# Kernel tuning notes

Measured on AMD Instinct MI355X. Metric: run time of the kernel, lower is better.

The kernel has to match this reference:

```python
import jax, jax.numpy as jnp
import numpy as np

NUM_EXPERTS = 64
TOP_K = 2
NOISE_EPS = 0.01


def setup_inputs() -> dict:
    key = jax.random.key(0)
    k1, k2, k3, k4 = jax.random.split(key, 4)
    B, D, E = 32768, 2048, NUM_EXPERTS
    x = jax.random.normal(k1, (B, D), dtype=jnp.float32)
    # original inits these to zero; use small random weights for a non-degenerate top-k
    w_gate = jax.random.normal(k2, (D, E), dtype=jnp.float32) * 0.02
    w_noise = jax.random.normal(k3, (D, E), dtype=jnp.float32) * 0.02
    noise = jax.random.normal(k4, (B, E), dtype=jnp.float32)  # tf.random.normal draw, fixed
    return {"x": x, "w_gate": w_gate, "w_noise": w_noise, "noise": noise}


def reference(x, w_gate, w_noise, noise):
    # routing_pooling='flatten' on a 2D input is identity
    pooled = x  # [B, D]
    routing = pooled @ w_gate  # [B, E]
    # noisy routing (training=True path)
    noise_stddev = jax.nn.softplus(pooled @ w_noise) + NOISE_EPS
    routing = routing + noise * noise_stddev
    # softmax_top_k: take top k+1, keep top k, softmax, scatter back to E experts
    kk = min(TOP_K + 1, NUM_EXPERTS)
    top_vals, top_idx = jax.lax.top_k(routing, kk)
    top_k_vals = top_vals[:, :TOP_K]            # [B, k]
    top_k_idx = top_idx[:, :TOP_K]              # [B, k]
    top_k_gates = jax.nn.softmax(top_k_vals, axis=-1)
    B = routing.shape[0]
    rows = jnp.arange(B)[:, None]
    # rowwise_unsorted_segment_sum -> scatter gates into expert slots
    out = jnp.zeros((B, NUM_EXPERTS), dtype=routing.dtype).at[rows, top_k_idx].add(top_k_gates)
    return out
```

## Files before the change

### kernel.cpp

```cpp
#include <hip/hip_runtime.h>
#include <math.h>


typedef _Float16 half8v __attribute__((ext_vector_type(8)));
typedef float f32x4  __attribute__((ext_vector_type(4)));
typedef float f32x16 __attribute__((ext_vector_type(16)));

constexpr int DIMK = 2048;
constexpr int NEXP = 64;
constexpr int BM   = 32;
constexpr int NCH  = DIMK / 32;

__device__ __forceinline__ void async_load16(const void* g, void* l) {
    __builtin_amdgcn_global_load_lds(
        (const __attribute__((address_space(1))) unsigned int*)g,
        (__attribute__((address_space(3))) unsigned int*)l, 16, 0, 0);
}

__device__ __forceinline__ bool gt_pair(float a, int ia, float b, int ib) {
    return (a > b) || (a == b && ia < ib);
}

__global__ __launch_bounds__(256)
void presplit_kernel(const float* __restrict__ wg, const float* __restrict__ wn,
                     _Float16* __restrict__ wsB)
{
    int gid  = blockIdx.x * 256 + threadIdx.x;
    int lane = gid & 63;
    int fb   = gid >> 6;
    int nt   = fb & 3;
    int p    = (fb >> 2) & 1;
    int kh   = (fb >> 3) & 1;
    int c    = fb >> 4;
    const float* src = (nt < 2) ? (wg + nt * 32 + (lane & 31))
                                : (wn + (nt - 2) * 32 + (lane & 31));
    int kb = c * 32 + kh * 16 + ((lane >> 5) << 3);
    half8v hp;
    #pragma unroll
    for (int j = 0; j < 8; ++j) {
        float w = src[(size_t)(kb + j) * NEXP] * 65536.0f;
        _Float16 a = (_Float16)w;
        hp[j] = p ? (_Float16)(w - (float)a) : a;
    }
    *(half8v*)(wsB + (size_t)fb * 512 + lane * 8) = hp;
}

__global__ __launch_bounds__(256, 4)
void routing_mfma(const float* __restrict__ x, const _Float16* __restrict__ wsB,
                  const float* __restrict__ noise, float* __restrict__ out)
{
    __shared__ _Float16 Bp[4][2][4][64][8];
    __shared__ float4   res[BM];

    const int tid  = threadIdx.x;
    const int lane = tid & 63;
    const int w    = tid >> 6;
    const int m    = lane & 31;
    const int h    = lane >> 5;
    const int row0 = blockIdx.x * BM;

    f32x16 acc = {};
    float4 ra[2][4];

    const float* xp = x + (size_t)(row0 + m) * DIMK + h * 8;

    auto issue_B = [&](int c, int buf) {
        #pragma unroll
        for (int kh = 0; kh < 2; ++kh)
            #pragma unroll
            for (int p = 0; p < 2; ++p) {
                int fb = c * 16 + kh * 8 + p * 4 + w;
                async_load16(wsB + (size_t)fb * 512 + lane * 8,
                             &Bp[w][buf][kh * 2 + p][0][0]);
            }
    };

#define ISSUE_X(C, S)                                            \
    {   const float* p_ = xp + (C) * 32;                         \
        ra[S][0] = *(const float4*)(p_);                         \
        ra[S][1] = *(const float4*)(p_ + 4);                     \
        ra[S][2] = *(const float4*)(p_ + 16);                    \
        ra[S][3] = *(const float4*)(p_ + 20);  }

#define FENCE() asm volatile("" ::: "memory")

#define STEP(C, SLOT, ISS, WN)                                               \
    {                                                                        \
        asm volatile("s_waitcnt vmcnt(" #WN ")" ::: "memory");               \
        half8v bf[2][2];                                                     \
        _Pragma("unroll")                                                    \
        for (int kh = 0; kh < 2; ++kh)                                       \
            _Pragma("unroll")                                                \
            for (int p = 0; p < 2; ++p)                                      \
                bf[kh][p] = *(const half8v*)&Bp[w][SLOT][kh * 2 + p][lane][0];\
        half8v afH[2], afL[2];                                               \
        _Pragma("unroll")                                                    \
        for (int kh = 0; kh < 2; ++kh) {                                     \
            float4 u = ra[SLOT][kh * 2];                                     \
            float4 v = ra[SLOT][kh * 2 + 1];                                 \
            float f0 = u.x * 1024.f, f1 = u.y * 1024.f;                      \
            float f2 = u.z * 1024.f, f3 = u.w * 1024.f;                      \
            float f4 = v.x * 1024.f, f5 = v.y * 1024.f;                      \
            float f6 = v.z * 1024.f, f7 = v.w * 1024.f;                      \
            _Float16 a0=(_Float16)f0, a1=(_Float16)f1, a2=(_Float16)f2,      \
                     a3=(_Float16)f3, a4=(_Float16)f4, a5=(_Float16)f5,      \
                     a6=(_Float16)f6, a7=(_Float16)f7;                       \
            afH[kh][0]=a0; afH[kh][1]=a1; afH[kh][2]=a2; afH[kh][3]=a3;      \
            afH[kh][4]=a4; afH[kh][5]=a5; afH[kh][6]=a6; afH[kh][7]=a7;      \
            afL[kh][0]=(_Float16)(f0-(float)a0);                             \
            afL[kh][1]=(_Float16)(f1-(float)a1);                             \
            afL[kh][2]=(_Float16)(f2-(float)a2);                             \
            afL[kh][3]=(_Float16)(f3-(float)a3);                             \
            afL[kh][4]=(_Float16)(f4-(float)a4);                             \
            afL[kh][5]=(_Float16)(f5-(float)a5);                             \
            afL[kh][6]=(_Float16)(f6-(float)a6);                             \
            afL[kh][7]=(_Float16)(f7-(float)a7);                             \
        }                                                                    \
        asm volatile("s_waitcnt lgkmcnt(0)" ::: "memory");                   \
        if (ISS) { issue_B((C) + 2, SLOT); ISSUE_X((C) + 2, SLOT); }         \
        __builtin_amdgcn_s_setprio(1);                                       \
        _Pragma("unroll")                                                    \
        for (int kh = 0; kh < 2; ++kh) {                                     \
            acc = __builtin_amdgcn_mfma_f32_32x32x16_f16(                    \
                afH[kh], bf[kh][0], acc, 0, 0, 0);                           \
            acc = __builtin_amdgcn_mfma_f32_32x32x16_f16(                    \
                afH[kh], bf[kh][1], acc, 0, 0, 0);                           \
            acc = __builtin_amdgcn_mfma_f32_32x32x16_f16(                    \
                afL[kh], bf[kh][0], acc, 0, 0, 0);                           \
        }                                                                    \
        __builtin_amdgcn_s_setprio(0);                                       \
    }

    issue_B(0, 0);
    ISSUE_X(0, 0);
    FENCE();
    issue_B(1, 1);
    ISSUE_X(1, 1);

    #pragma unroll 1
    for (int c = 0; c < NCH - 4; c += 2) {
        STEP(c + 0, 0, 1, 8)
        STEP(c + 1, 1, 1, 8)
    }
    STEP(NCH - 4, 0, 1, 8)
    STEP(NCH - 3, 1, 1, 8)
    STEP(NCH - 2, 0, 0, 8)
    STEP(NCH - 1, 1, 0, 0)

#undef STEP
#undef ISSUE_X
#undef FENCE

    const float s = 0x1p-26f;
    {
        float* scr = (float*)&Bp[w][0][0][0][0];
        #pragma unroll
        for (int reg = 0; reg < 16; ++reg) {
            int r = (reg & 3) + 8 * (reg >> 2) + 4 * h;
            scr[r * 33 + m] = acc[reg] * s;
        }
    }
    __syncthreads();

    {
        int r  = tid >> 3;
        int s8 = tid & 7;
        const float* gsrc = (const float*)&Bp[s8 >> 2][0][0][0][0];
        const float* nsrc = (const float*)&Bp[2 + (s8 >> 2)][0][0][0][0];
        int cs = (s8 * 8) & 31;
        float4 z0 = *(const float4*)(noise + (size_t)(row0 + r) * NEXP + s8 * 8);
        float4 z1 = *(const float4*)(noise + (size_t)(row0 + r) * NEXP + s8 * 8 + 4);
        float zz[8] = {z0.x, z0.y, z0.z, z0.w, z1.x, z1.y, z1.z, z1.w};
        float v1 = -INFINITY, v2 = -INFINITY; int i1 = 0x7ffffffe, i2 = 0x7fffffff;
        #pragma unroll
        for (int j = 0; j < 8; ++j) {
            float gate = gsrc[r * 33 + cs + j];
            float nv   = nsrc[r * 33 + cs + j];
            float sp   = fmaxf(nv, 0.f) + log1pf(expf(-fabsf(nv)));
            float vv   = gate + zz[j] * (sp + 0.01f);
            int   e    = s8 * 8 + j;
            if (gt_pair(vv, e, v1, i1)) { v2 = v1; i2 = i1; v1 = vv; i1 = e; }
            else if (gt_pair(vv, e, v2, i2)) { v2 = vv; i2 = e; }
        }
        #pragma unroll
        for (int mm = 1; mm <= 4; mm <<= 1) {
            float b1 = __shfl_xor(v1, mm); int ib1 = __shfl_xor(i1, mm);
            float b2 = __shfl_xor(v2, mm); int ib2 = __shfl_xor(i2, mm);
            if (gt_pair(b1, ib1, v1, i1)) {
                float o1 = v1; int oi1 = i1;
                v1 = b1; i1 = ib1;
                if (gt_pair(b2, ib2, o1, oi1)) { v2 = b2; i2 = ib2; }
                else                           { v2 = o1; i2 = oi1; }
            } else if (gt_pair(b1, ib1, v2, i2)) {
                v2 = b1; i2 = ib1;
            }
        }
        if (s8 == 0) {
            float t  = expf(v2 - v1);
            float g1 = 1.f / (1.f + t);
            res[r] = make_float4(g1, __int_as_float(i1),
                                 t * g1, __int_as_float(i2));
        }
    }
    __syncthreads();

    {
        int rr  = tid >> 3;
        int seg = tid & 7;
        float4 rv = res[rr];
        float g1 = rv.x, g2 = rv.z;
        int   j1 = __float_as_int(rv.y), j2 = __float_as_int(rv.w);
        float* op = out + (size_t)(row0 + rr) * NEXP + seg * 8;
        #pragma unroll
        for (int qq = 0; qq < 2; ++qq) {
            int e0 = seg * 8 + qq * 4;
            float4 o;
            o.x = (e0 + 0 == j1) ? g1 : ((e0 + 0 == j2) ? g2 : 0.f);
            o.y = (e0 + 1 == j1) ? g1 : ((e0 + 1 == j2) ? g2 : 0.f);
            o.z = (e0 + 2 == j1) ? g1 : ((e0 + 2 == j2) ? g2 : 0.f);
            o.w = (e0 + 3 == j1) ? g1 : ((e0 + 3 == j2) ? g2 : 0.f);
            *(float4*)(op + qq * 4) = o;
        }
    }
}

extern "C" void kernel_launch(void* const* d_in, const int* in_sizes, int n_in,
                              void* d_out, int out_size, void* d_ws, size_t ws_size,
                              hipStream_t stream) {
    const float* x     = (const float*)d_in[0];
    const float* wg    = (const float*)d_in[1];
    const float* wn    = (const float*)d_in[2];
    const float* noise = (const float*)d_in[3];
    float* out = (float*)d_out;
    _Float16* wsB = (_Float16*)d_ws;

    presplit_kernel<<<dim3(256), 256, 0, stream>>>(wg, wn, wsB);

    const int Brows = in_sizes[0] / DIMK;
    dim3 grid(Brows / BM);
    routing_mfma<<<grid, 256, 0, stream>>>(x, wsB, noise, out);
}
```

Baseline: 472.9 us.

## Stage x through swizzled LDS with 64-row, 512-thread blocks sharing B tiles

Doubles the row tile to 64 and the block to 8 waves. Each B chunk loaded into LDS is now reused by two row groups, and x is staged into LDS via async global_load_lds with an XOR swizzle instead of being loaded into registers. The hand-tuned vmcnt pipeline and priority hints are replaced by a plain double-buffered loop with a __syncthreads per chunk. The epilogue writes gates straight from the reducing lanes, dropping one barrier. Intended to halve B traffic per row and improve load coalescing, at the cost of a block-wide barrier every chunk and higher LDS use.

```diff
diff --git a/kernel.cpp b/kernel.cpp
--- a/kernel.cpp
+++ b/kernel.cpp
@@ -3,12 +3,11 @@
 
 
 typedef _Float16 half8v __attribute__((ext_vector_type(8)));
-typedef float f32x4  __attribute__((ext_vector_type(4)));
 typedef float f32x16 __attribute__((ext_vector_type(16)));
 
 constexpr int DIMK = 2048;
 constexpr int NEXP = 64;
-constexpr int BM   = 32;
+constexpr int BM   = 64;
 constexpr int NCH  = DIMK / 32;
 
 __device__ __forceinline__ void async_load16(const void* g, void* l) {
@@ -45,140 +44,128 @@
     *(half8v*)(wsB + (size_t)fb * 512 + lane * 8) = hp;
 }
 
-__global__ __launch_bounds__(256, 4)
+__global__ __launch_bounds__(512, 4)
 void routing_mfma(const float* __restrict__ x, const _Float16* __restrict__ wsB,
                   const float* __restrict__ noise, float* __restrict__ out)
 {
-    __shared__ _Float16 Bp[4][2][4][64][8];
-    __shared__ float4   res[BM];
+    __shared__ __align__(16) char smem[49152];
+    _Float16* Bs = (_Float16*)smem;
+    float*    Xs = (float*)(smem + 32768);
 
     const int tid  = threadIdx.x;
     const int lane = tid & 63;
     const int w    = tid >> 6;
+    const int rg   = w >> 2;
+    const int t    = w & 3;
     const int m    = lane & 31;
     const int h    = lane >> 5;
     const int row0 = blockIdx.x * BM;
 
     f32x16 acc = {};
-    float4 ra[2][4];
-
-    const float* xp = x + (size_t)(row0 + m) * DIMK + h * 8;
-
-    auto issue_B = [&](int c, int buf) {
-        #pragma unroll
-        for (int kh = 0; kh < 2; ++kh)
+
+    const int r7   = lane >> 3;
+    const int ssrc = (lane & 7) ^ (r7 & 7);
+    const float* xsrc = x + (size_t)(row0 + w * 8 + r7) * DIMK + ssrc * 4;
+
+    auto stage = [&](int c, int buf) {
+        #pragma unroll
+        for (int ii = 0; ii < 2; ++ii) {
+            int idx = w * 2 + ii;
+            async_load16(wsB + ((size_t)c * 16 + idx) * 512 + lane * 8,
+                         Bs + buf * 8192 + idx * 512);
+        }
+        async_load16(xsrc + c * 32, Xs + buf * 2048 + w * 256);
+    };
+
+    stage(0, 0);
+    stage(1, 1);
+    __syncthreads();
+
+    const int r   = rg * 32 + m;
+    const int rx7 = r & 7;
+
+    for (int c = 0; c < NCH; ++c) {
+        const int buf = c & 1;
+        const float*    xrow = Xs + buf * 2048 + r * 32;
+        const _Float16* bb   = Bs + buf * 8192 + t * 512 + lane * 8;
+
+        half8v bH0 = *(const half8v*)(bb);
+        half8v bL0 = *(const half8v*)(bb + 2048);
+        half8v bH1 = *(const half8v*)(bb + 4096);
+        half8v bL1 = *(const half8v*)(bb + 6144);
+
+        float4 x00 = *(const float4*)(xrow + ((h * 2 + 0) ^ rx7) * 4);
+        float4 x01 = *(const float4*)(xrow + ((h * 2 + 1) ^ rx7) * 4);
+        float4 x10 = *(const float4*)(xrow + ((4 + h * 2 + 0) ^ rx7) * 4);
+        float4 x11 = *(const float4*)(xrow + ((4 + h * 2 + 1) ^ rx7) * 4);
+
+        half8v aH0, aL0, aH1, aL1;
+        {
+            float f[8] = {x00.x, x00.y, x00.z, x00.w, x01.x, x01.y, x01.z, x01.w};
             #pragma unroll
-            for (int p = 0; p < 2; ++p) {
-                int fb = c * 16 + kh * 8 + p * 4 + w;
-                async_load16(wsB + (size_t)fb * 512 + lane * 8,
-                             &Bp[w][buf][kh * 2 + p][0][0]);
+            for (int j = 0; j < 8; ++j) {
+                float v = f[j] * 1024.f;
+                _Float16 a = (_Float16)v;
+                aH0[j] = a; aL0[j] = (_Float16)(v - (float)a);
             }
-    };
-
-#define ISSUE_X(C, S)                                            \
-    {   const float* p_ = xp + (C) * 32;                         \
-        ra[S][0] = *(const float4*)(p_);                         \
-        ra[S][1] = *(const float4*)(p_ + 4);                     \
-        ra[S][2] = *(const float4*)(p_ + 16);                    \
-        ra[S][3] = *(const float4*)(p_ + 20);  }
-
-#define FENCE() asm volatile("" ::: "memory")
-
-#define STEP(C, SLOT, ISS, WN)                                               \
-    {                                                                        \
-        asm volatile("s_waitcnt vmcnt(" #WN ")" ::: "memory");               \
-        half8v bf[2][2];                                                     \
-        _Pragma("unroll")                                                    \
-        for (int kh = 0; kh < 2; ++kh)                                       \
-            _Pragma("unroll")                                                \
-            for (int p = 0; p < 2; ++p)                                      \
-                bf[kh][p] = *(const half8v*)&Bp[w][SLOT][kh * 2 + p][lane][0];\
-        half8v afH[2], afL[2];                                               \
-        _Pragma("unroll")                                                    \
-        for (int kh = 0; kh < 2; ++kh) {                                     \
-            float4 u = ra[SLOT][kh * 2];                                     \
-            float4 v = ra[SLOT][kh * 2 + 1];                                 \
-            float f0 = u.x * 1024.f, f1 = u.y * 1024.f;                      \
-            float f2 = u.z * 1024.f, f3 = u.w * 1024.f;                      \
-            float f4 = v.x * 1024.f, f5 = v.y * 1024.f;                      \
-            float f6 = v.z * 1024.f, f7 = v.w * 1024.f;                      \
-            _Float16 a0=(_Float16)f0, a1=(_Float16)f1, a2=(_Float16)f2,      \
-                     a3=(_Float16)f3, a4=(_Float16)f4, a5=(_Float16)f5,      \
-                     a6=(_Float16)f6, a7=(_Float16)f7;                       \
-            afH[kh][0]=a0; afH[kh][1]=a1; afH[kh][2]=a2; afH[kh][3]=a3;      \
-            afH[kh][4]=a4; afH[kh][5]=a5; afH[kh][6]=a6; afH[kh][7]=a7;      \
-            afL[kh][0]=(_Float16)(f0-(float)a0);                             \
-            afL[kh][1]=(_Float16)(f1-(float)a1);                             \
-            afL[kh][2]=(_Float16)(f2-(float)a2);                             \
-            afL[kh][3]=(_Float16)(f3-(float)a3);                             \
-            afL[kh][4]=(_Float16)(f4-(float)a4);                             \
-            afL[kh][5]=(_Float16)(f5-(float)a5);                             \
-            afL[kh][6]=(_Float16)(f6-(float)a6);                             \
-            afL[kh][7]=(_Float16)(f7-(float)a7);                             \
-        }                                                                    \
-        asm volatile("s_waitcnt lgkmcnt(0)" ::: "memory");                   \
-        if (ISS) { issue_B((C) + 2, SLOT); ISSUE_X((C) + 2, SLOT); }         \
-        __builtin_amdgcn_s_setprio(1);                                       \
-        _Pragma("unroll")                                                    \
-        for (int kh = 0; kh < 2; ++kh) {                                     \
-            acc = __builtin_amdgcn_mfma_f32_32x32x16_f16(                    \
-                afH[kh], bf[kh][0], acc, 0, 0, 0);                           \
-            acc = __builtin_amdgcn_mfma_f32_32x32x16_f16(                    \
-                afH[kh], bf[kh][1], acc, 0, 0, 0);                           \
-            acc = __builtin_amdgcn_mfma_f32_32x32x16_f16(                    \
-                afL[kh], bf[kh][0], acc, 0, 0, 0);                           \
-        }                                                                    \
-        __builtin_amdgcn_s_setprio(0);                                       \
-    }
-
-    issue_B(0, 0);
-    ISSUE_X(0, 0);
-    FENCE();
-    issue_B(1, 1);
-    ISSUE_X(1, 1);
-
-    #pragma unroll 1
-    for (int c = 0; c < NCH - 4; c += 2) {
-        STEP(c + 0, 0, 1, 8)
-        STEP(c + 1, 1, 1, 8)
-    }
-    STEP(NCH - 4, 0, 1, 8)
-    STEP(NCH - 3, 1, 1, 8)
-    STEP(NCH - 2, 0, 0, 8)
-    STEP(NCH - 1, 1, 0, 0)
-
-#undef STEP
-#undef ISSUE_X
-#undef FENCE
+        }
+        {
+            float f[8] = {x10.x, x10.y, x10.z, x10.w, x11.x, x11.y, x11.z, x11.w};
+            #pragma unroll
+            for (int j = 0; j < 8; ++j) {
+                float v = f[j] * 1024.f;
+                _Float16 a = (_Float16)v;
+                aH1[j] = a; aL1[j] = (_Float16)(v - (float)a);
+            }
+        }
+
+        acc = __builtin_amdgcn_mfma_f32_32x32x16_f16(aH0, bH0, acc, 0, 0, 0);
+        acc = __builtin_amdgcn_mfma_f32_32x32x16_f16(aH0, bL0, acc, 0, 0, 0);
+        acc = __builtin_amdgcn_mfma_f32_32x32x16_f16(aL0, bH0, acc, 0, 0, 0);
+        acc = __builtin_amdgcn_mfma_f32_32x32x16_f16(aH1, bH1, acc, 0, 0, 0);
+        acc = __builtin_amdgcn_mfma_f32_32x32x16_f16(aH1, bL1, acc, 0, 0, 0);
+        acc = __builtin_amdgcn_mfma_f32_32x32x16_f16(aL1, bH1, acc, 0, 0, 0);
+
+        __syncthreads();
+        if (c + 2 < NCH) stage(c + 2, buf);
+    }
 
     const float s = 0x1p-26f;
+    constexpr int SLD = 68;
+    float* scr = (float*)smem;
     {
-        float* scr = (float*)&Bp[w][0][0][0][0];
+        const int pl   = (t >> 1) * 64 * SLD;
+        const int colb = (t & 1) * 32 + m;
         #pragma unroll
         for (int reg = 0; reg < 16; ++reg) {
-            int r = (reg & 3) + 8 * (reg >> 2) + 4 * h;
-            scr[r * 33 + m] = acc[reg] * s;
+            int rl = (reg & 3) + 8 * (reg >> 2) + 4 * h;
+            scr[pl + (rg * 32 + rl) * SLD + colb] = acc[reg] * s;
         }
     }
     __syncthreads();
 
     {
-        int r  = tid >> 3;
+        int rr = tid >> 3;
         int s8 = tid & 7;
-        const float* gsrc = (const float*)&Bp[s8 >> 2][0][0][0][0];
-        const float* nsrc = (const float*)&Bp[2 + (s8 >> 2)][0][0][0][0];
-        int cs = (s8 * 8) & 31;
-        float4 z0 = *(const float4*)(noise + (size_t)(row0 + r) * NEXP + s8 * 8);
-        float4 z1 = *(const float4*)(noise + (size_t)(row0 + r) * NEXP + s8 * 8 + 4);
+        const float* gp = scr + rr * SLD + s8 * 8;
+        const float* np = scr + 64 * SLD + rr * SLD + s8 * 8;
+        float4 g0 = *(const float4*)(gp);
+        float4 g1 = *(const float4*)(gp + 4);
+        float4 n0 = *(const float4*)(np);
+        float4 n1 = *(const float4*)(np + 4);
+        float4 z0 = *(const float4*)(noise + (size_t)(row0 + rr) * NEXP + s8 * 8);
+        float4 z1 = *(const float4*)(noise + (size_t)(row0 + rr) * NEXP + s8 * 8 + 4);
+        float gg[8] = {g0.x, g0.y, g0.z, g0.w, g1.x, g1.y, g1.z, g1.w};
+        float nn[8] = {n0.x, n0.y, n0.z, n0.w, n1.x, n1.y, n1.z, n1.w};
         float zz[8] = {z0.x, z0.y, z0.z, z0.w, z1.x, z1.y, z1.z, z1.w};
-        float v1 = -INFINITY, v2 = -INFINITY; int i1 = 0x7ffffffe, i2 = 0x7fffffff;
+        float v1 = -INFINITY, v2 = -INFINITY;
+        int   i1 = 0x7ffffffe,  i2 = 0x7fffffff;
         #pragma unroll
         for (int j = 0; j < 8; ++j) {
-            float gate = gsrc[r * 33 + cs + j];
-            float nv   = nsrc[r * 33 + cs + j];
-            float sp   = fmaxf(nv, 0.f) + log1pf(expf(-fabsf(nv)));
-            float vv   = gate + zz[j] * (sp + 0.01f);
-            int   e    = s8 * 8 + j;
+            float nv = nn[j];
+            float sp = fmaxf(nv, 0.f) + log1pf(expf(-fabsf(nv)));
+            float vv = gg[j] + zz[j] * (sp + 0.01f);
+            int   e  = s8 * 8 + j;
             if (gt_pair(vv, e, v1, i1)) { v2 = v1; i2 = i1; v1 = vv; i1 = e; }
             else if (gt_pair(vv, e, v2, i2)) { v2 = vv; i2 = e; }
         }
@@ -195,30 +182,18 @@
                 v2 = b1; i2 = ib1;
             }
         }
-        if (s8 == 0) {
-            float t  = expf(v2 - v1);
-            float g1 = 1.f / (1.f + t);
-            res[r] = make_float4(g1, __int_as_float(i1),
-                                 t * g1, __int_as_float(i2));
-        }
-    }
-    __syncthreads();
-
-    {
-        int rr  = tid >> 3;
-        int seg = tid & 7;
-        float4 rv = res[rr];
-        float g1 = rv.x, g2 = rv.z;
-        int   j1 = __float_as_int(rv.y), j2 = __float_as_int(rv.w);
-        float* op = out + (size_t)(row0 + rr) * NEXP + seg * 8;
+        float te = expf(v2 - v1);
+        float ga = 1.f / (1.f + te);
+        float gb = te * ga;
+        float* op = out + (size_t)(row0 + rr) * NEXP + s8 * 8;
         #pragma unroll
         for (int qq = 0; qq < 2; ++qq) {
-            int e0 = seg * 8 + qq * 4;
+            int e0 = s8 * 8 + qq * 4;
             float4 o;
-            o.x = (e0 + 0 == j1) ? g1 : ((e0 + 0 == j2) ? g2 : 0.f);
-            o.y = (e0 + 1 == j1) ? g1 : ((e0 + 1 == j2) ? g2 : 0.f);
-            o.z = (e0 + 2 == j1) ? g1 : ((e0 + 2 == j2) ? g2 : 0.f);
-            o.w = (e0 + 3 == j1) ? g1 : ((e0 + 3 == j2) ? g2 : 0.f);
+            o.x = (e0 + 0 == i1) ? ga : ((e0 + 0 == i2) ? gb : 0.f);
+            o.y = (e0 + 1 == i1) ? ga : ((e0 + 1 == i2) ? gb : 0.f);
+            o.z = (e0 + 2 == i1) ? ga : ((e0 + 2 == i2) ? gb : 0.f);
+            o.w = (e0 + 3 == i1) ? ga : ((e0 + 3 == i2) ? gb : 0.f);
             *(float4*)(op + qq * 4) = o;
         }
     }
@@ -238,5 +213,5 @@
 
     const int Brows = in_sizes[0] / DIMK;
     dim3 grid(Brows / BM);
-    routing_mfma<<<grid, 256, 0, stream>>>(x, wsB, noise, out);
-}
+    routing_mfma<<<grid, 512, 0, stream>>>(x, wsB, noise, out);
+}
```

Result: faster. 399.8 us (-15.5%).
